# Kernel optimization log

Hardware: AMD Instinct MI355X
Metric: run time of the kernel (lower is better)

## Reference

```python
import jax, jax.numpy as jnp
import numpy as np

T, B, H = 2048, 8, 1024


def setup_inputs() -> dict:
    key = jax.random.key(0)
    ks = jax.random.split(key, 4)
    scale = 1.0 / np.sqrt(H)
    x = jax.random.normal(ks[0], (T, B, H), dtype=jnp.float32)
    W_q = jax.random.normal(ks[1], (H, H), dtype=jnp.float32) * scale
    b_q = jnp.zeros((H,), dtype=jnp.float32)
    beta_raw = jax.random.normal(ks[2], (H,), dtype=jnp.float32)
    W_fc = jax.random.normal(ks[3], (H, H), dtype=jnp.float32) * scale
    b_fc = jnp.zeros((H,), dtype=jnp.float32)
    return {"x": x, "W_q": W_q, "b_q": b_q, "beta_raw": beta_raw,
            "W_fc": W_fc, "b_fc": b_fc}


def reference(x, W_q, b_q, beta_raw, W_fc, b_fc):
    # Per-neuron learned leak in (0,1)
    beta = jax.nn.sigmoid(beta_raw)  # (H,)
    # Input (q) projection: (T,B,H) @ (H,H)^T
    q = jnp.einsum('tbh,oh->tbo', x, W_q) + b_q  # (T,B,H)
    # Leaky integration m_t = beta * m_{t-1} + q_t as an associative scan over T
    a = jnp.broadcast_to(beta, q.shape)  # (T,B,H)

    def combine(c1, c2):
        a1, m1 = c1
        a2, m2 = c2
        return (a1 * a2, a2 * m1 + m2)

    _, m = jax.lax.associative_scan(combine, (a, q), axis=0)  # (T,B,H)
    # Linear + ReLU
    h = jnp.einsum('tbh,oh->tbo', m, W_fc) + b_fc
    return jax.nn.relu(h)
```

## Files before the change

### kernel.cpp

```cpp
#include <hip/hip_runtime.h>
#include <stdint.h>

typedef unsigned short u16;
typedef __bf16 bf16x8 __attribute__((ext_vector_type(8)));
typedef float f32x4 __attribute__((ext_vector_type(4)));

__device__ __forceinline__ u16 f2bf(float f) {
  union { float f; uint32_t u; } x; x.f = f;
  uint32_t u = x.u;
  u += 0x7fffu + ((u >> 16) & 1u);
  return (u16)(u >> 16);
}
__device__ __forceinline__ float bf2f(uint32_t lo16) {
  union { uint32_t u; float f; } x; x.u = lo16 << 16; return x.f;
}
__device__ __forceinline__ float bfhi(uint32_t u) {
  union { uint32_t u; float f; } x; x.u = u & 0xffff0000u; return x.f;
}
__device__ __forceinline__ uint32_t fixpair(uint32_t m, float p0, float p1,
                                            float F0, float F1) {
  float e0 = fmaf(p0, F0, bf2f(m & 0xffffu));
  float e1 = fmaf(p1, F1, bfhi(m));
  return (uint32_t)f2bf(e0) | ((uint32_t)f2bf(e1) << 16);
}

__device__ __forceinline__ void async_load16(const u16* g, u16* l) {
  __builtin_amdgcn_global_load_lds(
      (const __attribute__((address_space(1))) void*)g,
      (__attribute__((address_space(3))) void*)l,
      16, 0, 0);
}

__global__ __launch_bounds__(256) void prep_all(const float* __restrict__ x,
                                                const float* __restrict__ Wq,
                                                const float* __restrict__ Wfc,
                                                const float* __restrict__ braw,
                                                u16* __restrict__ xb,
                                                u16* __restrict__ wqb,
                                                u16* __restrict__ wfcb,
                                                float* __restrict__ beta,
                                                float* __restrict__ bpow) {
  int gid = blockIdx.x * 256 + threadIdx.x;
  if (gid < 1024) {
    float b = 1.0f / (1.0f + expf(-braw[gid]));
    beta[gid] = b;
    float w = b;
#pragma unroll 1
    for (int p = 1; p <= 32; p++) { bpow[p * 1024 + gid] = w; w *= b; }
  }
  if (gid < 131072) {
    const int HH = 1024 * 1024;
    int i = gid * 16;
    const float* src = (i < HH) ? (Wq + i) : (Wfc + (i - HH));
    u16* dst = (i < HH) ? (wqb + i) : (wfcb + (i - HH));
#pragma unroll
    for (int c = 0; c < 4; c++) {
      float4 v = *(const float4*)(src + c * 4);
      ushort4 o = {f2bf(v.x), f2bf(v.y), f2bf(v.z), f2bf(v.w)};
      *(ushort4*)(dst + c * 4) = o;
    }
  }
  {
    int i = gid * 8;
    float4 a = *(const float4*)(x + i);
    float4 b = *(const float4*)(x + i + 4);
    ushort4 o0 = {f2bf(a.x), f2bf(a.y), f2bf(a.z), f2bf(a.w)};
    ushort4 o1 = {f2bf(b.x), f2bf(b.y), f2bf(b.z), f2bf(b.w)};
    *(ushort4*)(xb + i) = o0;
    *(ushort4*)(xb + i + 4) = o1;
  }
}

__global__ __launch_bounds__(512, 2) void gemm_scan(const u16* __restrict__ A,
                                                    const u16* __restrict__ B,
                                                    const float* __restrict__ bias,
                                                    u16* __restrict__ Cout,
                                                    const float* __restrict__ beta_arr,
                                                    float* __restrict__ carry_out,
                                                    int M, int N, int K) {
  __shared__ u16 lds[4][2][256 * 32];

  const int tid  = threadIdx.x;
  const int lane = tid & 63;
  const int wid  = tid >> 6;
  const int wr   = (wid >> 2) * 128;
  const int wc   = (wid & 3) * 64;

  const int bid    = blockIdx.x;
  const int xcd    = bid & 7;
  const int idx    = bid >> 3;
  const int tile_m = ((xcd << 3) | (idx >> 2)) * 256;
  const int tile_n = (idx & 3) * 256;

  const int srow    = tid >> 2;
  const int schunk  = (tid & 3) ^ ((srow >> 1) & 3);
  const u16* gA = A + (size_t)(tile_m + srow) * K + schunk * 8;
  const u16* gB = B + (size_t)(tile_n + srow) * K + schunk * 8;
  const size_t half_stride = (size_t)128 * K;

#define STAGE(slot, kt)                                                   \
  do {                                                                    \
    const size_t k0 = (size_t)(kt) * 32;                                  \
    async_load16(gA + k0,               &lds[slot][0][wid * 512]);        \
    async_load16(gA + k0 + half_stride, &lds[slot][0][4096 + wid * 512]); \
    async_load16(gB + k0,               &lds[slot][1][wid * 512]);        \
    async_load16(gB + k0 + half_stride, &lds[slot][1][4096 + wid * 512]); \
  } while (0)

  f32x4 acc[8][4];
#pragma unroll
  for (int i = 0; i < 8; i++)
#pragma unroll
    for (int j = 0; j < 4; j++) acc[i][j] = (f32x4){0.f, 0.f, 0.f, 0.f};

  const int lrow = lane & 15;
  const int kq   = lane >> 4;
  const int kc   = (lrow >> 1) & 3;
  const int coff = ((kq ^ kc) << 3);

  const int NKT = K >> 5;

  STAGE(0, 0);
  if (NKT > 1) STAGE(1, 1);
  if (NKT > 2) STAGE(2, 2);
  if (NKT > 2)      asm volatile("s_waitcnt vmcnt(8)" ::: "memory");
  else if (NKT > 1) asm volatile("s_waitcnt vmcnt(4)" ::: "memory");
  else              asm volatile("s_waitcnt vmcnt(0)" ::: "memory");
  __builtin_amdgcn_s_barrier();

  for (int kt = 0; kt < NKT; ++kt) {
    const int slot = kt & 3;
    const u16* As = &lds[slot][0][0];
    const u16* Bs = &lds[slot][1][0];

    bf16x8 a[8], b[4];
#pragma unroll
    for (int i = 0; i < 8; i++)
      a[i] = *(const bf16x8*)&As[(wr + i * 16 + lrow) * 32 + coff];
#pragma unroll
    for (int j = 0; j < 4; j++)
      b[j] = *(const bf16x8*)&Bs[(wc + j * 16 + lrow) * 32 + coff];

    if (kt + 3 < NKT) STAGE((kt + 3) & 3, kt + 3);

    __builtin_amdgcn_s_setprio(1);
#pragma unroll
    for (int i = 0; i < 8; i++)
#pragma unroll
      for (int j = 0; j < 4; j++)
        acc[i][j] = __builtin_amdgcn_mfma_f32_16x16x32_bf16(a[i], b[j], acc[i][j], 0, 0, 0);
    __builtin_amdgcn_s_setprio(0);

    const int ahead = NKT - 1 - kt;
    if (ahead >= 3) {
      asm volatile("s_waitcnt vmcnt(8)" ::: "memory");
      __builtin_amdgcn_s_barrier();
    } else if (ahead == 2) {
      asm volatile("s_waitcnt vmcnt(4)" ::: "memory");
      __builtin_amdgcn_s_barrier();
    } else if (ahead == 1) {
      asm volatile("s_waitcnt vmcnt(0)" ::: "memory");
      __builtin_amdgcn_s_barrier();
    }
  }
#undef STAGE

  const int crow = (lane >> 4) << 2;
  const int ccol = lane & 15;
  const int c4   = lane >> 4;
  const int kap  = c4 >> 1;
  const int Wh   = wr >> 7;
  float* sm15 = (float*)&lds[0][0][0];

#pragma unroll
  for (int j = 0; j < 4; j++) {
    const int gn = tile_n + wc + j * 16 + ccol;
    const float bv = bias[gn];
    const float be = beta_arr[gn];
    const float be2 = be * be;
#pragma unroll
    for (int r = 0; r < 4; r++) {
      float S[8], R[8];
      S[0] = acc[0][j][r] + bv;
#pragma unroll
      for (int i = 1; i < 8; i++) S[i] = fmaf(be2, S[i - 1], acc[i][j][r] + bv);
#pragma unroll
      for (int i = 0; i < 8; i++) R[i] = __shfl_xor(S[i], 32);
      acc[0][j][r] = kap ? fmaf(be, R[0], S[0]) : S[0];
#pragma unroll
      for (int i = 1; i < 8; i++)
        acc[i][j][r] = fmaf(be, kap ? R[i] : R[i - 1], S[i]);
    }
  }
  if (Wh == 0 && kap == 1) {
#pragma unroll
    for (int j = 0; j < 4; j++)
#pragma unroll
      for (int r = 0; r < 4; r++) {
        const int bb = ((c4 << 2) + r) & 7;
        sm15[bb * 256 + wc + j * 16 + ccol] = acc[7][j][r];
      }
  }
  __syncthreads();
  if (Wh == 1) {
#pragma unroll
    for (int j = 0; j < 4; j++) {
      const int hl = wc + j * 16 + ccol;
      const float be = beta_arr[tile_n + hl];
      const float be2 = be * be;
#pragma unroll
      for (int r = 0; r < 4; r++) {
        const int bb = ((c4 << 2) + r) & 7;
        const float v = sm15[bb * 256 + hl];
        float f = kap ? be2 : be;
#pragma unroll
        for (int i = 0; i < 8; i++) {
          acc[i][j][r] = fmaf(f, v, acc[i][j][r]);
          f *= be2;
        }
      }
    }
  }
#pragma unroll
  for (int i = 0; i < 8; i++) {
#pragma unroll
    for (int j = 0; j < 4; j++) {
      const int gm = tile_m + wr + i * 16 + crow;
      const int gn = tile_n + wc + j * 16 + ccol;
#pragma unroll
      for (int r = 0; r < 4; r++)
        Cout[(size_t)(gm + r) * N + gn] = f2bf(acc[i][j][r]);
    }
  }
  if (Wh == 1 && kap == 1) {
    const int seg = tile_m >> 8;
#pragma unroll
    for (int j = 0; j < 4; j++) {
      const int hl = wc + j * 16 + ccol;
#pragma unroll
      for (int r = 0; r < 4; r++) {
        const int bb = ((c4 << 2) + r) & 7;
        carry_out[(size_t)seg * 8192 + bb * 1024 + tile_n + hl] = acc[7][j][r];
      }
    }
  }
}

__global__ __launch_bounds__(256) void ffold(const float4* __restrict__ carry4,
                                             const float* __restrict__ bpow,
                                             float4* __restrict__ Fbuf) {
  const int cq = blockIdx.x * 256 + threadIdx.x;
  const int hq = cq & 255;
  const float4 b32 = *(const float4*)&bpow[32 * 1024 + hq * 4];
  float4 F = make_float4(0.f, 0.f, 0.f, 0.f);
  for (int s = 0; s < 64; s++) {
    Fbuf[(size_t)s * 2048 + cq] = F;
    float4 c = carry4[(size_t)s * 2048 + cq];
    F.x = fmaf(b32.x, F.x, c.x);
    F.y = fmaf(b32.y, F.y, c.y);
    F.z = fmaf(b32.z, F.z, c.z);
    F.w = fmaf(b32.w, F.w, c.w);
  }
}

__global__ __launch_bounds__(512, 1) void gemm_fix(const u16* __restrict__ A,
                                                   const u16* __restrict__ B,
                                                   const float* __restrict__ bias,
                                                   float* __restrict__ Cout,
                                                   const float* __restrict__ bpow,
                                                   const float* __restrict__ Fbuf,
                                                   int M, int N, int K) {
  __shared__ u16 lds[4][2][256 * 32];

  const int tid  = threadIdx.x;
  const int lane = tid & 63;
  const int wid  = tid >> 6;
  const int wr   = (wid >> 2) * 128;
  const int wc   = (wid & 3) * 64;

  const int bid    = blockIdx.x;
  const int xcd    = bid & 7;
  const int idx    = bid >> 3;
  const int tile_m = ((xcd << 3) | (idx >> 2)) * 256;
  const int tile_n = (idx & 3) * 256;

  const int srow    = tid >> 2;
  const int schunk  = (tid & 3) ^ ((srow >> 1) & 3);
  const int t0      = srow >> 3;
  const int bb      = srow & 7;
  const int seg     = tile_m >> 8;

  const u16*   gA2 = A + (size_t)(tile_m + srow) * K + schunk * 8;
  const u16*   gB  = B + (size_t)(tile_n + srow) * K + schunk * 8;
  const float* pb0 = bpow + (size_t)(t0 + 1) * 1024 + schunk * 8;
  const float* fb0 = Fbuf + (size_t)seg * 8192 + bb * 1024 + schunk * 8;
  const size_t half_stride = (size_t)128 * K;

  struct ARegs { uint4 m0, m1; float4 p0l, p0h, p1l, p1h, fl, fh; };
  ARegs R;

#define STAGE_B2(slot, kt)                                                \
  do {                                                                    \
    const size_t k0 = (size_t)(kt) * 32;                                  \
    async_load16(gB + k0,               &lds[slot][1][wid * 512]);        \
    async_load16(gB + k0 + half_stride, &lds[slot][1][4096 + wid * 512]); \
  } while (0)

#define LOADA(kt)                                                         \
  do {                                                                    \
    const size_t o = (size_t)(kt) * 32;                                   \
    R.m0  = *(const uint4*)(gA2 + o);                                     \
    R.m1  = *(const uint4*)(gA2 + o + half_stride);                       \
    R.p0l = *(const float4*)(pb0 + o);                                    \
    R.p0h = *(const float4*)(pb0 + o + 4);                                \
    R.p1l = *(const float4*)(pb0 + o + 16384);                            \
    R.p1h = *(const float4*)(pb0 + o + 16388);                            \
    R.fl  = *(const float4*)(fb0 + o);                                    \
    R.fh  = *(const float4*)(fb0 + o + 4);                                \
  } while (0)

#define FIXWRITE(slot)                                                    \
  do {                                                                    \
    uint4 w0, w1;                                                         \
    w0.x = fixpair(R.m0.x, R.p0l.x, R.p0l.y, R.fl.x, R.fl.y);             \
    w0.y = fixpair(R.m0.y, R.p0l.z, R.p0l.w, R.fl.z, R.fl.w);             \
    w0.z = fixpair(R.m0.z, R.p0h.x, R.p0h.y, R.fh.x, R.fh.y);             \
    w0.w = fixpair(R.m0.w, R.p0h.z, R.p0h.w, R.fh.z, R.fh.w);             \
    w1.x = fixpair(R.m1.x, R.p1l.x, R.p1l.y, R.fl.x, R.fl.y);             \
    w1.y = fixpair(R.m1.y, R.p1l.z, R.p1l.w, R.fl.z, R.fl.w);             \
    w1.z = fixpair(R.m1.z, R.p1h.x, R.p1h.y, R.fh.x, R.fh.y);             \
    w1.w = fixpair(R.m1.w, R.p1h.z, R.p1h.w, R.fh.z, R.fh.w);             \
    *(uint4*)&lds[slot][0][tid * 8]        = w0;                          \
    *(uint4*)&lds[slot][0][4096 + tid * 8] = w1;                          \
  } while (0)

  f32x4 acc[8][4];
#pragma unroll
  for (int i = 0; i < 8; i++)
#pragma unroll
    for (int j = 0; j < 4; j++) acc[i][j] = (f32x4){0.f, 0.f, 0.f, 0.f};

  const int lrow = lane & 15;
  const int kq   = lane >> 4;
  const int kc   = (lrow >> 1) & 3;
  const int coff = ((kq ^ kc) << 3);

  const int NKT = K >> 5;

  STAGE_B2(0, 0);
  STAGE_B2(1, 1);
  STAGE_B2(2, 2);
  LOADA(0);
  asm volatile("s_waitcnt vmcnt(0)" ::: "memory");
  FIXWRITE(0);
  LOADA(1);
  asm volatile("s_waitcnt vmcnt(0)" ::: "memory");
  FIXWRITE(1);
  LOADA(2);
  asm volatile("s_waitcnt lgkmcnt(0)" ::: "memory");
  __builtin_amdgcn_sched_barrier(0);
  __builtin_amdgcn_s_barrier();

  for (int kt = 0; kt < NKT; ++kt) {
    const int slot = kt & 3;
    bf16x8 a[8], b[4];
#pragma unroll
    for (int i = 0; i < 8; i++)
      a[i] = *(const bf16x8*)&lds[slot][0][(wr + i * 16 + lrow) * 32 + coff];
#pragma unroll
    for (int j = 0; j < 4; j++)
      b[j] = *(const bf16x8*)&lds[slot][1][(wc + j * 16 + lrow) * 32 + coff];

    if (kt + 3 < NKT) STAGE_B2((kt + 3) & 3, kt + 3);
    __builtin_amdgcn_sched_barrier(0);
    if (kt + 2 < NKT) {
      if (kt + 3 < NKT) asm volatile("s_waitcnt vmcnt(2)" ::: "memory");
      else              asm volatile("s_waitcnt vmcnt(0)" ::: "memory");
      FIXWRITE((kt + 2) & 3);
    }
    if (kt + 3 < NKT) LOADA(kt + 3);
    __builtin_amdgcn_sched_barrier(0);

    __builtin_amdgcn_s_setprio(1);
#pragma unroll
    for (int i = 0; i < 8; i++)
#pragma unroll
      for (int j = 0; j < 4; j++)
        acc[i][j] = __builtin_amdgcn_mfma_f32_16x16x32_bf16(a[i], b[j], acc[i][j], 0, 0, 0);
    __builtin_amdgcn_s_setprio(0);

    if (kt < NKT - 1) {
      asm volatile("s_waitcnt lgkmcnt(0)" ::: "memory");
      __builtin_amdgcn_sched_barrier(0);
      __builtin_amdgcn_s_barrier();
    }
  }
#undef FIXWRITE
#undef LOADA
#undef STAGE_B2

  const int crow = (lane >> 4) << 2;
  const int ccol = lane & 15;
#pragma unroll
  for (int i = 0; i < 8; i++) {
#pragma unroll
    for (int j = 0; j < 4; j++) {
      const int gm = tile_m + wr + i * 16 + crow;
      const int gn = tile_n + wc + j * 16 + ccol;
      const float bv = bias[gn];
#pragma unroll
      for (int r = 0; r < 4; r++) {
        float v = acc[i][j][r] + bv;
        v = fmaxf(v, 0.f);
        Cout[(size_t)(gm + r) * N + gn] = v;
      }
    }
  }
}

extern "C" void kernel_launch(void* const* d_in, const int* in_sizes, int n_in,
                              void* d_out, int out_size, void* d_ws, size_t ws_size,
                              hipStream_t stream) {
  const float* x        = (const float*)d_in[0];
  const float* W_q      = (const float*)d_in[1];
  const float* b_q      = (const float*)d_in[2];
  const float* beta_raw = (const float*)d_in[3];
  const float* W_fc     = (const float*)d_in[4];
  const float* b_fc     = (const float*)d_in[5];

  const int H = 1024;
  const int M = 2048 * 8;
  const size_t MH = (size_t)M * H;

  char* ws = (char*)d_ws;
  u16* x_bf    = (u16*)ws;  ws += MH * 2;
  u16* m_loc   = (u16*)ws;  ws += MH * 2;
  u16* wq_bf   = (u16*)ws;  ws += (size_t)H * H * 2;
  u16* wfc_bf  = (u16*)ws;  ws += (size_t)H * H * 2;
  float* beta  = (float*)ws; ws += 4096;
  float* bpow  = (float*)ws; ws += 33 * 1024 * 4;
  float* carry = (float*)ws; ws += (size_t)64 * 8192 * 4;
  float* Fbuf  = (float*)ws; ws += (size_t)64 * 8192 * 4;

  prep_all<<<(int)(MH / 8 / 256), 256, 0, stream>>>(x, W_q, W_fc, beta_raw,
                                                    x_bf, wq_bf, wfc_bf, beta, bpow);

  gemm_scan<<<256, 512, 0, stream>>>(x_bf, wq_bf, b_q, m_loc, beta, carry, M, H, H);

  ffold<<<8, 256, 0, stream>>>((const float4*)carry, bpow, (float4*)Fbuf);

  gemm_fix<<<256, 512, 0, stream>>>(m_loc, wfc_bf, b_fc, (float*)d_out,
                                    bpow, Fbuf, M, H, H);
}
```

Before: 237.6 us.

## Fuse carry fold into gemm_fix prologue and reorder MFMA before fix writes

Removes the separate ffold kernel; each gemm_fix block now serially folds the carries of all preceding segments into Fbuf for its own segment before the main loop. This saves a kernel launch and a serialization point, but adds redundant per-block work whose length grows with segment index. The MFMA block is also moved ahead of the A-fixup writes and the priority hints removed, changing the overlap of compute with the fixup loads.

```diff
diff --git a/kernel.cpp b/kernel.cpp
--- a/kernel.cpp
+++ b/kernel.cpp
@@ -246,29 +246,13 @@
   }
 }
 
-__global__ __launch_bounds__(256) void ffold(const float4* __restrict__ carry4,
-                                             const float* __restrict__ bpow,
-                                             float4* __restrict__ Fbuf) {
-  const int cq = blockIdx.x * 256 + threadIdx.x;
-  const int hq = cq & 255;
-  const float4 b32 = *(const float4*)&bpow[32 * 1024 + hq * 4];
-  float4 F = make_float4(0.f, 0.f, 0.f, 0.f);
-  for (int s = 0; s < 64; s++) {
-    Fbuf[(size_t)s * 2048 + cq] = F;
-    float4 c = carry4[(size_t)s * 2048 + cq];
-    F.x = fmaf(b32.x, F.x, c.x);
-    F.y = fmaf(b32.y, F.y, c.y);
-    F.z = fmaf(b32.z, F.z, c.z);
-    F.w = fmaf(b32.w, F.w, c.w);
-  }
-}
-
 __global__ __launch_bounds__(512, 1) void gemm_fix(const u16* __restrict__ A,
                                                    const u16* __restrict__ B,
                                                    const float* __restrict__ bias,
                                                    float* __restrict__ Cout,
                                                    const float* __restrict__ bpow,
-                                                   const float* __restrict__ Fbuf,
+                                                   const float* __restrict__ carry,
+                                                   float* __restrict__ Fbuf,
                                                    int M, int N, int K) {
   __shared__ u16 lds[4][2][256 * 32];
 
@@ -295,6 +279,39 @@
   const float* pb0 = bpow + (size_t)(t0 + 1) * 1024 + schunk * 8;
   const float* fb0 = Fbuf + (size_t)seg * 8192 + bb * 1024 + schunk * 8;
   const size_t half_stride = (size_t)128 * K;
+
+  {
+    const int fb  = tid >> 6;
+    const int h0  = (tid & 63) << 4;
+    const float4 w0 = *(const float4*)&bpow[32 * 1024 + h0 + 0];
+    const float4 w1 = *(const float4*)&bpow[32 * 1024 + h0 + 4];
+    const float4 w2 = *(const float4*)&bpow[32 * 1024 + h0 + 8];
+    const float4 w3 = *(const float4*)&bpow[32 * 1024 + h0 + 12];
+    float4 F0 = {0.f, 0.f, 0.f, 0.f}, F1 = F0, F2 = F0, F3 = F0;
+    const float* cb = carry + fb * 1024 + h0;
+#pragma unroll 1
+    for (int s = 0; s < seg; s++) {
+      const float4 c0 = *(const float4*)&cb[(size_t)s * 8192 + 0];
+      const float4 c1 = *(const float4*)&cb[(size_t)s * 8192 + 4];
+      const float4 c2 = *(const float4*)&cb[(size_t)s * 8192 + 8];
+      const float4 c3 = *(const float4*)&cb[(size_t)s * 8192 + 12];
+      F0.x = fmaf(w0.x, F0.x, c0.x); F0.y = fmaf(w0.y, F0.y, c0.y);
+      F0.z = fmaf(w0.z, F0.z, c0.z); F0.w = fmaf(w0.w, F0.w, c0.w);
+      F1.x = fmaf(w1.x, F1.x, c1.x); F1.y = fmaf(w1.y, F1.y, c1.y);
+      F1.z = fmaf(w1.z, F1.z, c1.z); F1.w = fmaf(w1.w, F1.w, c1.w);
+      F2.x = fmaf(w2.x, F2.x, c2.x); F2.y = fmaf(w2.y, F2.y, c2.y);
+      F2.z = fmaf(w2.z, F2.z, c2.z); F2.w = fmaf(w2.w, F2.w, c2.w);
+      F3.x = fmaf(w3.x, F3.x, c3.x); F3.y = fmaf(w3.y, F3.y, c3.y);
+      F3.z = fmaf(w3.z, F3.z, c3.z); F3.w = fmaf(w3.w, F3.w, c3.w);
+    }
+    float* fo = Fbuf + (size_t)seg * 8192 + fb * 1024 + h0;
+    *(float4*)&fo[0]  = F0;
+    *(float4*)&fo[4]  = F1;
+    *(float4*)&fo[8]  = F2;
+    *(float4*)&fo[12] = F3;
+  }
+  asm volatile("s_waitcnt vmcnt(0)" ::: "memory");
+  __syncthreads();
 
   struct ARegs { uint4 m0, m1; float4 p0l, p0h, p1l, p1h, fl, fh; };
   ARegs R;
@@ -373,21 +390,20 @@
 
     if (kt + 3 < NKT) STAGE_B2((kt + 3) & 3, kt + 3);
     __builtin_amdgcn_sched_barrier(0);
+
+#pragma unroll
+    for (int i = 0; i < 8; i++)
+#pragma unroll
+      for (int j = 0; j < 4; j++)
+        acc[i][j] = __builtin_amdgcn_mfma_f32_16x16x32_bf16(a[i], b[j], acc[i][j], 0, 0, 0);
+
     if (kt + 2 < NKT) {
       if (kt + 3 < NKT) asm volatile("s_waitcnt vmcnt(2)" ::: "memory");
       else              asm volatile("s_waitcnt vmcnt(0)" ::: "memory");
+      __builtin_amdgcn_sched_barrier(0);
       FIXWRITE((kt + 2) & 3);
     }
     if (kt + 3 < NKT) LOADA(kt + 3);
-    __builtin_amdgcn_sched_barrier(0);
-
-    __builtin_amdgcn_s_setprio(1);
-#pragma unroll
-    for (int i = 0; i < 8; i++)
-#pragma unroll
-      for (int j = 0; j < 4; j++)
-        acc[i][j] = __builtin_amdgcn_mfma_f32_16x16x32_bf16(a[i], b[j], acc[i][j], 0, 0, 0);
-    __builtin_amdgcn_s_setprio(0);
 
     if (kt < NKT - 1) {
       asm volatile("s_waitcnt lgkmcnt(0)" ::: "memory");
@@ -447,8 +463,6 @@
 
   gemm_scan<<<256, 512, 0, stream>>>(x_bf, wq_bf, b_q, m_loc, beta, carry, M, H, H);
 
-  ffold<<<8, 256, 0, stream>>>((const float4*)carry, bpow, (float4*)Fbuf);
-
   gemm_fix<<<256, 512, 0, stream>>>(m_loc, wfc_bf, b_fc, (float*)d_out,
-                                    bpow, Fbuf, M, H, H);
-}
+                                    bpow, carry, Fbuf, M, H, H);
+}
```

After: 249.5 us. 5.0% more time.

## Split scan carry fixup out of second GEMM into standalone elementwise kernel

Applied to the files above, without the earlier changes.

The cross-segment carry correction that was fused into the A-tile load of the second GEMM now runs in its own elementwise kernel, which writes a corrected bf16 buffer. The GEMM then loads both A and B asynchronously straight into LDS with a simple multi-stage vmcnt pipeline and no register-staged fixup. This removes the VGPR pressure and scheduling stalls of the fused fixup, and the launch bounds now allow two blocks per CU. The cost is an extra 32 MB read and 32 MB write of the m buffer plus one more kernel launch.

```diff
diff --git a/kernel.cpp b/kernel.cpp
--- a/kernel.cpp
+++ b/kernel.cpp
@@ -263,13 +263,38 @@
   }
 }
 
-__global__ __launch_bounds__(512, 1) void gemm_fix(const u16* __restrict__ A,
-                                                   const u16* __restrict__ B,
-                                                   const float* __restrict__ bias,
-                                                   float* __restrict__ Cout,
-                                                   const float* __restrict__ bpow,
-                                                   const float* __restrict__ Fbuf,
-                                                   int M, int N, int K) {
+__global__ __launch_bounds__(256) void mfix(const uint4* __restrict__ mloc,
+                                            const float* __restrict__ bpow,
+                                            const float* __restrict__ Fbuf,
+                                            uint4* __restrict__ mout) {
+  const int stride = gridDim.x * 256;
+  const int total  = 16384 * 128;
+  for (int idx = blockIdx.x * 256 + threadIdx.x; idx < total; idx += stride) {
+    const int r   = idx >> 7;
+    const int hq  = idx & 127;
+    const int seg = r >> 8;
+    const int rl  = r & 255;
+    const int tl  = rl >> 3;
+    const int b   = rl & 7;
+    const float* p = bpow + (size_t)(tl + 1) * 1024 + hq * 8;
+    const float* f = Fbuf + (size_t)seg * 8192 + b * 1024 + hq * 8;
+    const float4 p0 = *(const float4*)p,       p1 = *(const float4*)(p + 4);
+    const float4 f0 = *(const float4*)f,       f1 = *(const float4*)(f + 4);
+    const uint4 m = mloc[idx];
+    uint4 o;
+    o.x = fixpair(m.x, p0.x, p0.y, f0.x, f0.y);
+    o.y = fixpair(m.y, p0.z, p0.w, f0.z, f0.w);
+    o.z = fixpair(m.z, p1.x, p1.y, f1.x, f1.y);
+    o.w = fixpair(m.w, p1.z, p1.w, f1.z, f1.w);
+    mout[idx] = o;
+  }
+}
+
+__global__ __launch_bounds__(512, 2) void gemm_relu(const u16* __restrict__ A,
+                                                    const u16* __restrict__ B,
+                                                    const float* __restrict__ bias,
+                                                    float* __restrict__ Cout,
+                                                    int M, int N, int K) {
   __shared__ u16 lds[4][2][256 * 32];
 
   const int tid  = threadIdx.x;
@@ -286,52 +311,17 @@
 
   const int srow    = tid >> 2;
   const int schunk  = (tid & 3) ^ ((srow >> 1) & 3);
-  const int t0      = srow >> 3;
-  const int bb      = srow & 7;
-  const int seg     = tile_m >> 8;
-
-  const u16*   gA2 = A + (size_t)(tile_m + srow) * K + schunk * 8;
-  const u16*   gB  = B + (size_t)(tile_n + srow) * K + schunk * 8;
-  const float* pb0 = bpow + (size_t)(t0 + 1) * 1024 + schunk * 8;
-  const float* fb0 = Fbuf + (size_t)seg * 8192 + bb * 1024 + schunk * 8;
+  const u16* gA = A + (size_t)(tile_m + srow) * K + schunk * 8;
+  const u16* gB = B + (size_t)(tile_n + srow) * K + schunk * 8;
   const size_t half_stride = (size_t)128 * K;
 
-  struct ARegs { uint4 m0, m1; float4 p0l, p0h, p1l, p1h, fl, fh; };
-  ARegs R;
-
-#define STAGE_B2(slot, kt)                                                \
+#define STAGE(slot, kt)                                                   \
   do {                                                                    \
     const size_t k0 = (size_t)(kt) * 32;                                  \
+    async_load16(gA + k0,               &lds[slot][0][wid * 512]);        \
+    async_load16(gA + k0 + half_stride, &lds[slot][0][4096 + wid * 512]); \
     async_load16(gB + k0,               &lds[slot][1][wid * 512]);        \
     async_load16(gB + k0 + half_stride, &lds[slot][1][4096 + wid * 512]); \
-  } while (0)
-
-#define LOADA(kt)                                                         \
-  do {                                                                    \
-    const size_t o = (size_t)(kt) * 32;                                   \
-    R.m0  = *(const uint4*)(gA2 + o);                                     \
-    R.m1  = *(const uint4*)(gA2 + o + half_stride);                       \
-    R.p0l = *(const float4*)(pb0 + o);                                    \
-    R.p0h = *(const float4*)(pb0 + o + 4);                                \
-    R.p1l = *(const float4*)(pb0 + o + 16384);                            \
-    R.p1h = *(const float4*)(pb0 + o + 16388);                            \
-    R.fl  = *(const float4*)(fb0 + o);                                    \
-    R.fh  = *(const float4*)(fb0 + o + 4);                                \
-  } while (0)
-
-#define FIXWRITE(slot)                                                    \
-  do {                                                                    \
-    uint4 w0, w1;                                                         \
-    w0.x = fixpair(R.m0.x, R.p0l.x, R.p0l.y, R.fl.x, R.fl.y);             \
-    w0.y = fixpair(R.m0.y, R.p0l.z, R.p0l.w, R.fl.z, R.fl.w);             \
-    w0.z = fixpair(R.m0.z, R.p0h.x, R.p0h.y, R.fh.x, R.fh.y);             \
-    w0.w = fixpair(R.m0.w, R.p0h.z, R.p0h.w, R.fh.z, R.fh.w);             \
-    w1.x = fixpair(R.m1.x, R.p1l.x, R.p1l.y, R.fl.x, R.fl.y);             \
-    w1.y = fixpair(R.m1.y, R.p1l.z, R.p1l.w, R.fl.z, R.fl.w);             \
-    w1.z = fixpair(R.m1.z, R.p1h.x, R.p1h.y, R.fh.x, R.fh.y);             \
-    w1.w = fixpair(R.m1.w, R.p1h.z, R.p1h.w, R.fh.z, R.fh.w);             \
-    *(uint4*)&lds[slot][0][tid * 8]        = w0;                          \
-    *(uint4*)&lds[slot][0][4096 + tid * 8] = w1;                          \
   } while (0)
 
   f32x4 acc[8][4];
@@ -347,39 +337,28 @@
 
   const int NKT = K >> 5;
 
-  STAGE_B2(0, 0);
-  STAGE_B2(1, 1);
-  STAGE_B2(2, 2);
-  LOADA(0);
-  asm volatile("s_waitcnt vmcnt(0)" ::: "memory");
-  FIXWRITE(0);
-  LOADA(1);
-  asm volatile("s_waitcnt vmcnt(0)" ::: "memory");
-  FIXWRITE(1);
-  LOADA(2);
-  asm volatile("s_waitcnt lgkmcnt(0)" ::: "memory");
-  __builtin_amdgcn_sched_barrier(0);
+  STAGE(0, 0);
+  if (NKT > 1) STAGE(1, 1);
+  if (NKT > 2) STAGE(2, 2);
+  if (NKT > 2)      asm volatile("s_waitcnt vmcnt(8)" ::: "memory");
+  else if (NKT > 1) asm volatile("s_waitcnt vmcnt(4)" ::: "memory");
+  else              asm volatile("s_waitcnt vmcnt(0)" ::: "memory");
   __builtin_amdgcn_s_barrier();
 
   for (int kt = 0; kt < NKT; ++kt) {
     const int slot = kt & 3;
+    const u16* As = &lds[slot][0][0];
+    const u16* Bs = &lds[slot][1][0];
+
     bf16x8 a[8], b[4];
 #pragma unroll
     for (int i = 0; i < 8; i++)
-      a[i] = *(const bf16x8*)&lds[slot][0][(wr + i * 16 + lrow) * 32 + coff];
+      a[i] = *(const bf16x8*)&As[(wr + i * 16 + lrow) * 32 + coff];
 #pragma unroll
     for (int j = 0; j < 4; j++)
-      b[j] = *(const bf16x8*)&lds[slot][1][(wc + j * 16 + lrow) * 32 + coff];
-
-    if (kt + 3 < NKT) STAGE_B2((kt + 3) & 3, kt + 3);
-    __builtin_amdgcn_sched_barrier(0);
-    if (kt + 2 < NKT) {
-      if (kt + 3 < NKT) asm volatile("s_waitcnt vmcnt(2)" ::: "memory");
-      else              asm volatile("s_waitcnt vmcnt(0)" ::: "memory");
-      FIXWRITE((kt + 2) & 3);
-    }
-    if (kt + 3 < NKT) LOADA(kt + 3);
-    __builtin_amdgcn_sched_barrier(0);
+      b[j] = *(const bf16x8*)&Bs[(wc + j * 16 + lrow) * 32 + coff];
+
+    if (kt + 3 < NKT) STAGE((kt + 3) & 3, kt + 3);
 
     __builtin_amdgcn_s_setprio(1);
 #pragma unroll
@@ -389,15 +368,19 @@
         acc[i][j] = __builtin_amdgcn_mfma_f32_16x16x32_bf16(a[i], b[j], acc[i][j], 0, 0, 0);
     __builtin_amdgcn_s_setprio(0);
 
-    if (kt < NKT - 1) {
-      asm volatile("s_waitcnt lgkmcnt(0)" ::: "memory");
-      __builtin_amdgcn_sched_barrier(0);
-      __builtin_amdgcn_s_barrier();
-    }
-  }
-#undef FIXWRITE
-#undef LOADA
-#undef STAGE_B2
+    const int ahead = NKT - 1 - kt;
+    if (ahead >= 3) {
+      asm volatile("s_waitcnt vmcnt(8)" ::: "memory");
+      __builtin_amdgcn_s_barrier();
+    } else if (ahead == 2) {
+      asm volatile("s_waitcnt vmcnt(4)" ::: "memory");
+      __builtin_amdgcn_s_barrier();
+    } else if (ahead == 1) {
+      asm volatile("s_waitcnt vmcnt(0)" ::: "memory");
+      __builtin_amdgcn_s_barrier();
+    }
+  }
+#undef STAGE
 
   const int crow = (lane >> 4) << 2;
   const int ccol = lane & 15;
@@ -435,6 +418,7 @@
   char* ws = (char*)d_ws;
   u16* x_bf    = (u16*)ws;  ws += MH * 2;
   u16* m_loc   = (u16*)ws;  ws += MH * 2;
+  u16* m_fix   = (u16*)ws;  ws += MH * 2;
   u16* wq_bf   = (u16*)ws;  ws += (size_t)H * H * 2;
   u16* wfc_bf  = (u16*)ws;  ws += (size_t)H * H * 2;
   float* beta  = (float*)ws; ws += 4096;
@@ -449,6 +433,7 @@
 
   ffold<<<8, 256, 0, stream>>>((const float4*)carry, bpow, (float4*)Fbuf);
 
-  gemm_fix<<<256, 512, 0, stream>>>(m_loc, wfc_bf, b_fc, (float*)d_out,
-                                    bpow, Fbuf, M, H, H);
-}
+  mfix<<<2048, 256, 0, stream>>>((const uint4*)m_loc, bpow, Fbuf, (uint4*)m_fix);
+
+  gemm_relu<<<256, 512, 0, stream>>>(m_fix, wfc_bf, b_fc, (float*)d_out, M, H, H);
+}
```

New measurement: 240.8 us. About the same (+1.3%).
